# Kernel optimization log

Hardware: AMD Instinct MI355X
Metric: run time of the kernel (lower is better)

## Reference

```python
import jax, jax.numpy as jnp
import numpy as np

N = 50000      # nodes
E = 640000     # edges (before self loops)
IN = 128       # in_channels
H = 4          # heads (layer 1)
C = 64         # hidden_channels per head
OUT = 64       # out_channels
SLOPE = 0.2    # PyG GATConv default negative_slope


def setup_inputs() -> dict:
    key = jax.random.key(0)
    ks = jax.random.split(key, 12)
    x = jax.random.normal(ks[0], (N, IN), dtype=jnp.float32)
    edge_src = jax.random.randint(ks[1], (E,), 0, N, dtype=jnp.int32)
    edge_dst = jax.random.randint(ks[2], (E,), 0, N, dtype=jnp.int32)
    # Layer 1 params: Linear IN -> H*C, attention vectors a_src/a_dst [H, C], bias [H*C]
    W1 = jax.random.normal(ks[3], (IN, H * C), dtype=jnp.float32) / np.sqrt(IN)
    att_src1 = jax.random.normal(ks[4], (H, C), dtype=jnp.float32) / np.sqrt(C)
    att_dst1 = jax.random.normal(ks[5], (H, C), dtype=jnp.float32) / np.sqrt(C)
    b1 = jnp.zeros((H * C,), dtype=jnp.float32)
    # Layer 2 params: Linear H*C -> OUT, 1 head
    W2 = jax.random.normal(ks[6], (H * C, OUT), dtype=jnp.float32) / np.sqrt(H * C)
    att_src2 = jax.random.normal(ks[7], (1, OUT), dtype=jnp.float32) / np.sqrt(OUT)
    att_dst2 = jax.random.normal(ks[8], (1, OUT), dtype=jnp.float32) / np.sqrt(OUT)
    b2 = jnp.zeros((OUT,), dtype=jnp.float32)
    return {"x": x, "W1": W1, "att_src1": att_src1, "att_dst1": att_dst1, "b1": b1,
            "W2": W2, "att_src2": att_src2, "att_dst2": att_dst2, "b2": b2,
            "edge_src": edge_src, "edge_dst": edge_dst}


def gat_conv(x, src, dst, W, a_src, a_dst, b, heads, ch):
    """PyG GATConv (concat=True): gather -> LeakyReLU attention -> per-dst softmax -> scatter-add."""
    n = x.shape[0]
    h = (x @ W).reshape(n, heads, ch)                  # [N, H, C]
    al_s = jnp.sum(h * a_src, axis=-1)                 # [N, H] node-level src attention term
    al_d = jnp.sum(h * a_dst, axis=-1)                 # [N, H]
    e = jax.nn.leaky_relu(al_s[src] + al_d[dst], SLOPE)  # [E, H] edge scores
    m = jax.ops.segment_max(e, dst, num_segments=n)    # stable per-dst softmax
    ex = jnp.exp(e - m[dst])
    den = jax.ops.segment_sum(ex, dst, num_segments=n)
    alpha = ex / den[dst]                              # [E, H]
    msg = h[src] * alpha[:, :, None]                   # [E, H, C]
    out = jax.ops.segment_sum(msg, dst, num_segments=n)  # [N, H, C]
    return out.reshape(n, heads * ch) + b


def reference(x, W1, att_src1, att_dst1, b1, W2, att_src2, att_dst2, b2, edge_src, edge_dst):
    # PyG GATConv default add_self_loops=True
    loops = jnp.arange(N, dtype=edge_src.dtype)
    src = jnp.concatenate([edge_src, loops])
    dst = jnp.concatenate([edge_dst, loops])
    h = gat_conv(x, src, dst, W1, att_src1, att_dst1, b1, H, C)
    h = jax.nn.elu(h)                                  # F.elu; dropout p=0 -> no-op
    out = gat_conv(h, src, dst, W2, att_src2, att_dst2, b2, 1, OUT)
    return out
```

## Files before the change

kernel.cpp:

```cpp
#include <hip/hip_runtime.h>
#include <hip/hip_bf16.h>
#include <cstdint>
#include <cstddef>

#define N_NODES 50000
#define N_EDGES 640000
#define ET (N_EDGES + N_NODES)
#define IN_CH 128
#define H1 4
#define HC1 256
#define OUT_CH 64
#define SLOPE 0.2f
#define SCAN_NBLK ((N_NODES + 255) / 256)

typedef __attribute__((ext_vector_type(8))) short short8;
typedef __attribute__((ext_vector_type(4))) float floatx4;

__device__ __forceinline__ float bf2f(unsigned short u) {
    return __uint_as_float(((unsigned)u) << 16);
}
__device__ __forceinline__ unsigned short f2bf(float f) {
    unsigned u = __float_as_uint(f);
    unsigned r = 0x7fffu + ((u >> 16) & 1u);
    return (unsigned short)((u + r) >> 16);
}
__device__ __forceinline__ float ldf(const void* p, size_t i, bool f32) {
    return f32 ? ((const float*)p)[i] : bf2f(((const unsigned short*)p)[i]);
}

__global__ void detect_dtype(const unsigned short* __restrict__ x, unsigned* __restrict__ flag) {
    if (blockIdx.x == 0 && threadIdx.x == 0) {
        int bad = 0;
        for (int i = 0; i < 256; ++i) {
            float v = bf2f(x[i]);
            if (!(v == v) || fabsf(v) > 1e4f) bad++;
        }
        *flag = (bad > 0) ? 1u : 0u;
    }
}

__global__ void conv_x(const void* __restrict__ x, const unsigned* __restrict__ flag,
                       unsigned short* __restrict__ x16)
{
    int i = blockIdx.x * blockDim.x + threadIdx.x;
    if (i >= N_NODES * IN_CH / 8) return;
    size_t off = (size_t)i * 8;
    uint4 st;
    if (*flag) {
        const float* xp = (const float*)x + off;
        float4 a = *(const float4*)xp;
        float4 b = *(const float4*)(xp + 4);
        st.x = (unsigned)f2bf(a.x) | ((unsigned)f2bf(a.y) << 16);
        st.y = (unsigned)f2bf(a.z) | ((unsigned)f2bf(a.w) << 16);
        st.z = (unsigned)f2bf(b.x) | ((unsigned)f2bf(b.y) << 16);
        st.w = (unsigned)f2bf(b.z) | ((unsigned)f2bf(b.w) << 16);
    } else {
        st = *(const uint4*)((const unsigned short*)x + off);
    }
    *(uint4*)(x16 + off) = st;
}

__global__ void conv_w(const void* __restrict__ W, const unsigned* __restrict__ flag,
                       unsigned short* __restrict__ Wt, int K, int N)
{
    int i = blockIdx.x * blockDim.x + threadIdx.x;
    if (i >= N * K) return;
    int n = i / K, k = i % K;
    Wt[i] = f2bf(ldf(W, (size_t)k * N + n, *flag != 0));
}

__global__ void count_edges(const int* __restrict__ edst, int* __restrict__ counts)
{
    int i = blockIdx.x * blockDim.x + threadIdx.x;
    if (i >= ET) return;
    int d = (i < N_EDGES) ? edst[i] : (i - N_EDGES);
    atomicAdd(&counts[d], 1);
}

__global__ __launch_bounds__(256) void block_sums(
    const int* __restrict__ counts, int* __restrict__ bsum)
{
    int i = blockIdx.x * 256 + threadIdx.x;
    int v = (i < N_NODES) ? counts[i] : 0;
    #pragma unroll
    for (int off = 32; off > 0; off >>= 1) v += __shfl_down(v, off, 64);
    __shared__ int ws[4];
    int lane = threadIdx.x & 63, w = threadIdx.x >> 6;
    if (lane == 0) ws[w] = v;
    __syncthreads();
    if (threadIdx.x == 0) bsum[blockIdx.x] = ws[0] + ws[1] + ws[2] + ws[3];
}

__global__ __launch_bounds__(256) void scan_block_sums(
    const int* __restrict__ bsum, int* __restrict__ boff)
{
    __shared__ int s[256];
    int t = threadIdx.x;
    int v = (t < SCAN_NBLK) ? bsum[t] : 0;
    s[t] = v;
    __syncthreads();
    #pragma unroll
    for (int off = 1; off < 256; off <<= 1) {
        int u = (t >= off) ? s[t - off] : 0;
        __syncthreads();
        s[t] += u;
        __syncthreads();
    }
    if (t < SCAN_NBLK) boff[t] = s[t] - v;
}

__global__ __launch_bounds__(256) void write_rowptr(
    const int* __restrict__ counts, const int* __restrict__ boff,
    int* __restrict__ rowptr, int* __restrict__ cursor)
{
    __shared__ int s[256];
    int t = threadIdx.x;
    int i = blockIdx.x * 256 + t;
    int v = (i < N_NODES) ? counts[i] : 0;
    s[t] = v;
    __syncthreads();
    #pragma unroll
    for (int off = 1; off < 256; off <<= 1) {
        int u = (t >= off) ? s[t - off] : 0;
        __syncthreads();
        s[t] += u;
        __syncthreads();
    }
    if (i < N_NODES) {
        int r = boff[blockIdx.x] + s[t] - v;
        rowptr[i] = r; cursor[i] = r;
    }
    if (i == 0) rowptr[N_NODES] = ET;
}

__global__ void fill_csr(const int* __restrict__ esrc, const int* __restrict__ edst,
                         int* __restrict__ cursor, int* __restrict__ ecsr)
{
    int i = blockIdx.x * blockDim.x + threadIdx.x;
    if (i >= ET) return;
    int s = (i < N_EDGES) ? esrc[i] : (i - N_EDGES);
    int d = (i < N_EDGES) ? edst[i] : (i - N_EDGES);
    int pos = atomicAdd(&cursor[d], 1);
    ecsr[pos] = s;
}

template <int KK>
__global__ __launch_bounds__(256) void gemm_fused(
    const unsigned short* __restrict__ A,
    const unsigned short* __restrict__ Bt,
    const void* __restrict__ avs, const void* __restrict__ avd,
    const unsigned* __restrict__ flag,
    unsigned short* __restrict__ C,
    float* __restrict__ als, float* __restrict__ ald,
    int M, int N)
{
    const int tid = threadIdx.x;
    const int m0 = blockIdx.y * 64, n0 = blockIdx.x * 64;
    const int w = tid >> 6, lane = tid & 63;
    const int ln = lane & 15, quad = lane >> 4;
    const int m_frag = m0 + w * 16 + ln;
    floatx4 acc[4] = {{0.f,0.f,0.f,0.f},{0.f,0.f,0.f,0.f},{0.f,0.f,0.f,0.f},{0.f,0.f,0.f,0.f}};

    #pragma unroll
    for (int ks = 0; ks < KK / 32; ++ks) {
        const int kbase = ks * 32 + quad * 8;
        short8 a;
        if (m_frag < M) {
            a = *(const short8*)(A + (size_t)m_frag * KK + kbase);
        } else {
            #pragma unroll
            for (int j = 0; j < 8; ++j) a[j] = 0;
        }
        #pragma unroll
        for (int sub = 0; sub < 4; ++sub) {
            short8 b = *(const short8*)(Bt + (size_t)(n0 + sub * 16 + ln) * KK + kbase);
            acc[sub] = __builtin_amdgcn_mfma_f32_16x16x32_bf16(a, b, acc[sub], 0, 0, 0);
        }
    }

    #pragma unroll
    for (int sub = 0; sub < 4; ++sub) {
        #pragma unroll
        for (int r = 0; r < 4; ++r) {
            int m = m0 + w * 16 + quad * 4 + r;
            if (m < M)
                C[(size_t)m * N + n0 + sub * 16 + ln] = f2bf(acc[sub][r]);
        }
    }

    const bool f32in = (*flag != 0);
    float as[4], av[4];
    #pragma unroll
    for (int sub = 0; sub < 4; ++sub) {
        as[sub] = ldf(avs, n0 + sub * 16 + ln, f32in);
        av[sub] = ldf(avd, n0 + sub * 16 + ln, f32in);
    }
    const int Hh = N >> 6;
    #pragma unroll
    for (int r = 0; r < 4; ++r) {
        float ps = 0.f, pd = 0.f;
        #pragma unroll
        for (int sub = 0; sub < 4; ++sub) {
            ps += acc[sub][r] * as[sub];
            pd += acc[sub][r] * av[sub];
        }
        #pragma unroll
        for (int off = 1; off < 16; off <<= 1) {
            ps += __shfl_xor(ps, off, 64);
            pd += __shfl_xor(pd, off, 64);
        }
        int m = m0 + w * 16 + quad * 4 + r;
        if (ln == 0 && m < M) {
            als[(size_t)m * Hh + blockIdx.x] = ps;
            ald[(size_t)m * Hh + blockIdx.x] = pd;
        }
    }
}

__global__ __launch_bounds__(256) void agg_node1(
    const int* __restrict__ rowptr, const int* __restrict__ ecsr,
    const unsigned short* __restrict__ h, const float* __restrict__ als,
    const float* __restrict__ ald, const void* __restrict__ bias,
    const unsigned* __restrict__ flag, unsigned short* __restrict__ out)
{
    int wave = (blockIdx.x * blockDim.x + threadIdx.x) >> 6;
    int lane = threadIdx.x & 63;
    if (wave >= N_NODES) return;
    const int d = wave;
    const int hg = lane >> 4;
    const int c0 = (lane & 15) << 2;
    const int lo = rowptr[d], hi = rowptr[d + 1];
    const float ad = ald[d * H1 + hg];

    float acc0 = 0.f, acc1 = 0.f, acc2 = 0.f, acc3 = 0.f, den = 0.f;

    int e = lo;
    for (; e + 1 < hi; e += 2) {
        int s0 = ecsr[e], s1 = ecsr[e + 1];
        uint2 q0 = *(const uint2*)(h + (size_t)s0 * HC1 + hg * 64 + c0);
        uint2 q1 = *(const uint2*)(h + (size_t)s1 * HC1 + hg * 64 + c0);
        float t0 = als[s0 * H1 + hg] + ad;
        float t1 = als[s1 * H1 + hg] + ad;
        t0 = (t0 > 0.f) ? t0 : SLOPE * t0;
        t1 = (t1 > 0.f) ? t1 : SLOPE * t1;
        float p0 = __expf(t0), p1 = __expf(t1);
        den += p0 + p1;
        acc0 += p0 * __uint_as_float(q0.x << 16)         + p1 * __uint_as_float(q1.x << 16);
        acc1 += p0 * __uint_as_float(q0.x & 0xffff0000u) + p1 * __uint_as_float(q1.x & 0xffff0000u);
        acc2 += p0 * __uint_as_float(q0.y << 16)         + p1 * __uint_as_float(q1.y << 16);
        acc3 += p0 * __uint_as_float(q0.y & 0xffff0000u) + p1 * __uint_as_float(q1.y & 0xffff0000u);
    }
    if (e < hi) {
        int s0 = ecsr[e];
        uint2 q0 = *(const uint2*)(h + (size_t)s0 * HC1 + hg * 64 + c0);
        float t0 = als[s0 * H1 + hg] + ad;
        t0 = (t0 > 0.f) ? t0 : SLOPE * t0;
        float p0 = __expf(t0);
        den += p0;
        acc0 += p0 * __uint_as_float(q0.x << 16);
        acc1 += p0 * __uint_as_float(q0.x & 0xffff0000u);
        acc2 += p0 * __uint_as_float(q0.y << 16);
        acc3 += p0 * __uint_as_float(q0.y & 0xffff0000u);
    }

    const bool f32in = (*flag != 0);
    const float inv = 1.f / den;
    float v0 = acc0 * inv + ldf(bias, hg * 64 + c0 + 0, f32in);
    float v1 = acc1 * inv + ldf(bias, hg * 64 + c0 + 1, f32in);
    float v2 = acc2 * inv + ldf(bias, hg * 64 + c0 + 2, f32in);
    float v3 = acc3 * inv + ldf(bias, hg * 64 + c0 + 3, f32in);
    v0 = (v0 > 0.f) ? v0 : (__expf(v0) - 1.f);
    v1 = (v1 > 0.f) ? v1 : (__expf(v1) - 1.f);
    v2 = (v2 > 0.f) ? v2 : (__expf(v2) - 1.f);
    v3 = (v3 > 0.f) ? v3 : (__expf(v3) - 1.f);
    uint2 st;
    st.x = (unsigned)f2bf(v0) | ((unsigned)f2bf(v1) << 16);
    st.y = (unsigned)f2bf(v2) | ((unsigned)f2bf(v3) << 16);
    *(uint2*)(out + (size_t)d * HC1 + hg * 64 + c0) = st;
}

__global__ __launch_bounds__(256) void agg_node2(
    const int* __restrict__ rowptr, const int* __restrict__ ecsr,
    const unsigned short* __restrict__ h, const float* __restrict__ als,
    const float* __restrict__ ald, const void* __restrict__ bias,
    const unsigned* __restrict__ flag, float* __restrict__ out)
{
    int wave = (blockIdx.x * blockDim.x + threadIdx.x) >> 6;
    int lane = threadIdx.x & 63;
    if (wave >= N_NODES) return;
    const int d = wave;
    const int eg = lane >> 4;
    const int c0 = (lane & 15) << 2;
    const int lo = rowptr[d], hi = rowptr[d + 1];
    const float ad = ald[d];

    float acc0 = 0.f, acc1 = 0.f, acc2 = 0.f, acc3 = 0.f, den = 0.f;

    for (int eb = lo; eb < hi; eb += 4) {
        int e = eb + eg;
        if (e < hi) {
            int s = ecsr[e];
            uint2 q = *(const uint2*)(h + (size_t)s * OUT_CH + c0);
            float t = als[s] + ad;
            t = (t > 0.f) ? t : SLOPE * t;
            float p = __expf(t);
            den += p;
            acc0 += p * __uint_as_float(q.x << 16);
            acc1 += p * __uint_as_float(q.x & 0xffff0000u);
            acc2 += p * __uint_as_float(q.y << 16);
            acc3 += p * __uint_as_float(q.y & 0xffff0000u);
        }
    }
    #pragma unroll
    for (int off = 16; off <= 32; off <<= 1) {
        den  += __shfl_xor(den,  off, 64);
        acc0 += __shfl_xor(acc0, off, 64);
        acc1 += __shfl_xor(acc1, off, 64);
        acc2 += __shfl_xor(acc2, off, 64);
        acc3 += __shfl_xor(acc3, off, 64);
    }
    if (lane < 16) {
        const bool f32in = (*flag != 0);
        const float inv = 1.f / den;
        float4 v;
        v.x = acc0 * inv + ldf(bias, c0 + 0, f32in);
        v.y = acc1 * inv + ldf(bias, c0 + 1, f32in);
        v.z = acc2 * inv + ldf(bias, c0 + 2, f32in);
        v.w = acc3 * inv + ldf(bias, c0 + 3, f32in);
        *(float4*)(out + (size_t)d * OUT_CH + c0) = v;
    }
}

extern "C" void kernel_launch(void* const* d_in, const int* in_sizes, int n_in,
                              void* d_out, int out_size, void* d_ws, size_t ws_size,
                              hipStream_t stream)
{
    const void* x   = d_in[0];
    const void* W1  = d_in[1];
    const void* as1 = d_in[2];
    const void* ad1 = d_in[3];
    const void* b1  = d_in[4];
    const void* W2  = d_in[5];
    const void* as2 = d_in[6];
    const void* ad2 = d_in[7];
    const void* b2  = d_in[8];
    const int* esrc = (const int*)d_in[9];
    const int* edst = (const int*)d_in[10];
    float* out = (float*)d_out;

    char* base = (char*)d_ws;
    const size_t MB = 1024 * 1024;
    unsigned short* x16  = (unsigned short*)(base);
    unsigned short* h16  = (unsigned short*)(base + 13 * MB);
    unsigned short* xo16 = (unsigned short*)(base + 39 * MB);
    unsigned short* h2   = (unsigned short*)(base + 65 * MB);
    float* als    = (float*)(base + 72 * MB);
    float* ald    = (float*)(base + 73 * MB);
    unsigned short* Wt1 = (unsigned short*)(base + 74 * MB);
    unsigned short* Wt2 = (unsigned short*)(base + 75 * MB);
    int* counts   = (int*)(base + 76 * MB);
    int* rowptr   = (int*)(base + 77 * MB);
    int* cursor   = (int*)(base + 78 * MB);
    int* ecsr     = (int*)(base + 79 * MB);
    int* bsum     = (int*)(base + 82 * MB);
    int* boff     = bsum + 256;
    unsigned* flag = (unsigned*)(base + 83 * MB);

    const int BLK = 256;
    const int edge_blocks = (ET + BLK - 1) / BLK;
    const int node_wave_blocks = (N_NODES * 64 + BLK - 1) / BLK;

    detect_dtype<<<1, 64, 0, stream>>>((const unsigned short*)x, flag);

    (void)hipMemsetAsync(counts, 0, N_NODES * sizeof(int), stream);
    count_edges<<<edge_blocks, BLK, 0, stream>>>(edst, counts);
    block_sums<<<SCAN_NBLK, BLK, 0, stream>>>(counts, bsum);
    scan_block_sums<<<1, BLK, 0, stream>>>(bsum, boff);
    write_rowptr<<<SCAN_NBLK, BLK, 0, stream>>>(counts, boff, rowptr, cursor);
    fill_csr<<<edge_blocks, BLK, 0, stream>>>(esrc, edst, cursor, ecsr);

    conv_x<<<(N_NODES * IN_CH / 8 + BLK - 1) / BLK, BLK, 0, stream>>>(x, flag, x16);
    conv_w<<<(IN_CH * HC1 + BLK - 1) / BLK, BLK, 0, stream>>>(W1, flag, Wt1, IN_CH, HC1);
    conv_w<<<(HC1 * OUT_CH + BLK - 1) / BLK, BLK, 0, stream>>>(W2, flag, Wt2, HC1, OUT_CH);

    {
        dim3 g(HC1 / 64, (N_NODES + 63) / 64);
        gemm_fused<IN_CH><<<g, BLK, 0, stream>>>(x16, Wt1, as1, ad1, flag, h16, als, ald, N_NODES, HC1);
    }
    agg_node1<<<node_wave_blocks, BLK, 0, stream>>>(
        rowptr, ecsr, h16, als, ald, b1, flag, xo16);

    {
        dim3 g(OUT_CH / 64, (N_NODES + 63) / 64);
        gemm_fused<HC1><<<g, BLK, 0, stream>>>(xo16, Wt2, as2, ad2, flag, h2, als, ald, N_NODES, OUT_CH);
    }
    agg_node2<<<node_wave_blocks, BLK, 0, stream>>>(
        rowptr, ecsr, h2, als, ald, b2, flag, out);
}
```

Baseline: 325.4 us.

## Compute all heads per GEMM block, unroll layer-1 aggregation, widen layer-2 loads

Layer-1 GEMM now runs one block per 64-row tile covering all four heads, so each A fragment is loaded once instead of once per column tile, at the cost of 64 accumulator registers per thread. The layer-1 aggregation loop is unrolled to four edges per iteration to keep more gathers in flight. Layer-2 aggregation switches to 8 edge groups of 8 lanes, each loading 16-byte rows, which adds one more shuffle reduction stage. The layer-2 GEMM drops its N-tiling parameters and becomes single-tile.

```diff
diff --git a/kernel.cpp b/kernel.cpp
--- a/kernel.cpp
+++ b/kernel.cpp
@@ -144,6 +144,91 @@
     ecsr[pos] = s;
 }
 
+__global__ __launch_bounds__(256) void gemm_fused4(
+    const unsigned short* __restrict__ A,
+    const unsigned short* __restrict__ Bt,
+    const void* __restrict__ avs, const void* __restrict__ avd,
+    const unsigned* __restrict__ flag,
+    unsigned short* __restrict__ C,
+    float* __restrict__ als, float* __restrict__ ald,
+    int M)
+{
+    const int tid = threadIdx.x;
+    const int m0 = blockIdx.x * 64;
+    const int w = tid >> 6, lane = tid & 63;
+    const int ln = lane & 15, quad = lane >> 4;
+    const int m_frag = m0 + w * 16 + ln;
+    floatx4 acc[4][4];
+    #pragma unroll
+    for (int hh = 0; hh < 4; ++hh)
+        #pragma unroll
+        for (int sub = 0; sub < 4; ++sub)
+            acc[hh][sub] = (floatx4){0.f, 0.f, 0.f, 0.f};
+
+    #pragma unroll
+    for (int ks = 0; ks < IN_CH / 32; ++ks) {
+        const int kbase = ks * 32 + quad * 8;
+        short8 a;
+        if (m_frag < M) {
+            a = *(const short8*)(A + (size_t)m_frag * IN_CH + kbase);
+        } else {
+            #pragma unroll
+            for (int j = 0; j < 8; ++j) a[j] = 0;
+        }
+        #pragma unroll
+        for (int hh = 0; hh < 4; ++hh) {
+            #pragma unroll
+            for (int sub = 0; sub < 4; ++sub) {
+                short8 b = *(const short8*)(Bt + (size_t)(hh * 64 + sub * 16 + ln) * IN_CH + kbase);
+                acc[hh][sub] = __builtin_amdgcn_mfma_f32_16x16x32_bf16(a, b, acc[hh][sub], 0, 0, 0);
+            }
+        }
+    }
+
+    #pragma unroll
+    for (int hh = 0; hh < 4; ++hh) {
+        #pragma unroll
+        for (int sub = 0; sub < 4; ++sub) {
+            #pragma unroll
+            for (int r = 0; r < 4; ++r) {
+                int m = m0 + w * 16 + quad * 4 + r;
+                if (m < M)
+                    C[(size_t)m * HC1 + hh * 64 + sub * 16 + ln] = f2bf(acc[hh][sub][r]);
+            }
+        }
+    }
+
+    const bool f32in = (*flag != 0);
+    #pragma unroll
+    for (int hh = 0; hh < 4; ++hh) {
+        float as[4], av[4];
+        #pragma unroll
+        for (int sub = 0; sub < 4; ++sub) {
+            as[sub] = ldf(avs, hh * 64 + sub * 16 + ln, f32in);
+            av[sub] = ldf(avd, hh * 64 + sub * 16 + ln, f32in);
+        }
+        #pragma unroll
+        for (int r = 0; r < 4; ++r) {
+            float ps = 0.f, pd = 0.f;
+            #pragma unroll
+            for (int sub = 0; sub < 4; ++sub) {
+                ps += acc[hh][sub][r] * as[sub];
+                pd += acc[hh][sub][r] * av[sub];
+            }
+            #pragma unroll
+            for (int off = 1; off < 16; off <<= 1) {
+                ps += __shfl_xor(ps, off, 64);
+                pd += __shfl_xor(pd, off, 64);
+            }
+            int m = m0 + w * 16 + quad * 4 + r;
+            if (ln == 0 && m < M) {
+                als[(size_t)m * H1 + hh] = ps;
+                ald[(size_t)m * H1 + hh] = pd;
+            }
+        }
+    }
+}
+
 template <int KK>
 __global__ __launch_bounds__(256) void gemm_fused(
     const unsigned short* __restrict__ A,
@@ -152,10 +237,10 @@
     const unsigned* __restrict__ flag,
     unsigned short* __restrict__ C,
     float* __restrict__ als, float* __restrict__ ald,
-    int M, int N)
+    int M)
 {
     const int tid = threadIdx.x;
-    const int m0 = blockIdx.y * 64, n0 = blockIdx.x * 64;
+    const int m0 = blockIdx.x * 64;
     const int w = tid >> 6, lane = tid & 63;
     const int ln = lane & 15, quad = lane >> 4;
     const int m_frag = m0 + w * 16 + ln;
@@ -173,7 +258,7 @@
         }
         #pragma unroll
         for (int sub = 0; sub < 4; ++sub) {
-            short8 b = *(const short8*)(Bt + (size_t)(n0 + sub * 16 + ln) * KK + kbase);
+            short8 b = *(const short8*)(Bt + (size_t)(sub * 16 + ln) * KK + kbase);
             acc[sub] = __builtin_amdgcn_mfma_f32_16x16x32_bf16(a, b, acc[sub], 0, 0, 0);
         }
     }
@@ -184,7 +269,7 @@
         for (int r = 0; r < 4; ++r) {
             int m = m0 + w * 16 + quad * 4 + r;
             if (m < M)
-                C[(size_t)m * N + n0 + sub * 16 + ln] = f2bf(acc[sub][r]);
+                C[(size_t)m * OUT_CH + sub * 16 + ln] = f2bf(acc[sub][r]);
         }
     }
 
@@ -192,10 +277,9 @@
     float as[4], av[4];
     #pragma unroll
     for (int sub = 0; sub < 4; ++sub) {
-        as[sub] = ldf(avs, n0 + sub * 16 + ln, f32in);
-        av[sub] = ldf(avd, n0 + sub * 16 + ln, f32in);
-    }
-    const int Hh = N >> 6;
+        as[sub] = ldf(avs, sub * 16 + ln, f32in);
+        av[sub] = ldf(avd, sub * 16 + ln, f32in);
+    }
     #pragma unroll
     for (int r = 0; r < 4; ++r) {
         float ps = 0.f, pd = 0.f;
@@ -211,8 +295,8 @@
         }
         int m = m0 + w * 16 + quad * 4 + r;
         if (ln == 0 && m < M) {
-            als[(size_t)m * Hh + blockIdx.x] = ps;
-            ald[(size_t)m * Hh + blockIdx.x] = pd;
+            als[m] = ps;
+            ald[m] = pd;
         }
     }
 }
@@ -235,22 +319,32 @@
     float acc0 = 0.f, acc1 = 0.f, acc2 = 0.f, acc3 = 0.f, den = 0.f;
 
     int e = lo;
-    for (; e + 1 < hi; e += 2) {
-        int s0 = ecsr[e], s1 = ecsr[e + 1];
+    for (; e + 3 < hi; e += 4) {
+        int s0 = ecsr[e], s1 = ecsr[e + 1], s2 = ecsr[e + 2], s3 = ecsr[e + 3];
         uint2 q0 = *(const uint2*)(h + (size_t)s0 * HC1 + hg * 64 + c0);
         uint2 q1 = *(const uint2*)(h + (size_t)s1 * HC1 + hg * 64 + c0);
+        uint2 q2 = *(const uint2*)(h + (size_t)s2 * HC1 + hg * 64 + c0);
+        uint2 q3 = *(const uint2*)(h + (size_t)s3 * HC1 + hg * 64 + c0);
         float t0 = als[s0 * H1 + hg] + ad;
         float t1 = als[s1 * H1 + hg] + ad;
+        float t2 = als[s2 * H1 + hg] + ad;
+        float t3 = als[s3 * H1 + hg] + ad;
         t0 = (t0 > 0.f) ? t0 : SLOPE * t0;
         t1 = (t1 > 0.f) ? t1 : SLOPE * t1;
-        float p0 = __expf(t0), p1 = __expf(t1);
-        den += p0 + p1;
-        acc0 += p0 * __uint_as_float(q0.x << 16)         + p1 * __uint_as_float(q1.x << 16);
-        acc1 += p0 * __uint_as_float(q0.x & 0xffff0000u) + p1 * __uint_as_float(q1.x & 0xffff0000u);
-        acc2 += p0 * __uint_as_float(q0.y << 16)         + p1 * __uint_as_float(q1.y << 16);
-        acc3 += p0 * __uint_as_float(q0.y & 0xffff0000u) + p1 * __uint_as_float(q1.y & 0xffff0000u);
-    }
-    if (e < hi) {
+        t2 = (t2 > 0.f) ? t2 : SLOPE * t2;
+        t3 = (t3 > 0.f) ? t3 : SLOPE * t3;
+        float p0 = __expf(t0), p1 = __expf(t1), p2 = __expf(t2), p3 = __expf(t3);
+        den += (p0 + p1) + (p2 + p3);
+        acc0 += p0 * __uint_as_float(q0.x << 16)         + p1 * __uint_as_float(q1.x << 16)
+              + p2 * __uint_as_float(q2.x << 16)         + p3 * __uint_as_float(q3.x << 16);
+        acc1 += p0 * __uint_as_float(q0.x & 0xffff0000u) + p1 * __uint_as_float(q1.x & 0xffff0000u)
+              + p2 * __uint_as_float(q2.x & 0xffff0000u) + p3 * __uint_as_float(q3.x & 0xffff0000u);
+        acc2 += p0 * __uint_as_float(q0.y << 16)         + p1 * __uint_as_float(q1.y << 16)
+              + p2 * __uint_as_float(q2.y << 16)         + p3 * __uint_as_float(q3.y << 16);
+        acc3 += p0 * __uint_as_float(q0.y & 0xffff0000u) + p1 * __uint_as_float(q1.y & 0xffff0000u)
+              + p2 * __uint_as_float(q2.y & 0xffff0000u) + p3 * __uint_as_float(q3.y & 0xffff0000u);
+    }
+    for (; e < hi; ++e) {
         int s0 = ecsr[e];
         uint2 q0 = *(const uint2*)(h + (size_t)s0 * HC1 + hg * 64 + c0);
         float t0 = als[s0 * H1 + hg] + ad;
@@ -289,45 +383,55 @@
     int lane = threadIdx.x & 63;
     if (wave >= N_NODES) return;
     const int d = wave;
-    const int eg = lane >> 4;
-    const int c0 = (lane & 15) << 2;
+    const int eg = lane >> 3;
+    const int c0 = (lane & 7) << 3;
     const int lo = rowptr[d], hi = rowptr[d + 1];
     const float ad = ald[d];
 
-    float acc0 = 0.f, acc1 = 0.f, acc2 = 0.f, acc3 = 0.f, den = 0.f;
-
-    for (int eb = lo; eb < hi; eb += 4) {
+    float acc[8];
+    #pragma unroll
+    for (int j = 0; j < 8; ++j) acc[j] = 0.f;
+    float den = 0.f;
+
+    for (int eb = lo; eb < hi; eb += 8) {
         int e = eb + eg;
         if (e < hi) {
             int s = ecsr[e];
-            uint2 q = *(const uint2*)(h + (size_t)s * OUT_CH + c0);
+            uint4 q = *(const uint4*)(h + (size_t)s * OUT_CH + c0);
             float t = als[s] + ad;
             t = (t > 0.f) ? t : SLOPE * t;
             float p = __expf(t);
             den += p;
-            acc0 += p * __uint_as_float(q.x << 16);
-            acc1 += p * __uint_as_float(q.x & 0xffff0000u);
-            acc2 += p * __uint_as_float(q.y << 16);
-            acc3 += p * __uint_as_float(q.y & 0xffff0000u);
-        }
-    }
-    #pragma unroll
-    for (int off = 16; off <= 32; off <<= 1) {
-        den  += __shfl_xor(den,  off, 64);
-        acc0 += __shfl_xor(acc0, off, 64);
-        acc1 += __shfl_xor(acc1, off, 64);
-        acc2 += __shfl_xor(acc2, off, 64);
-        acc3 += __shfl_xor(acc3, off, 64);
-    }
-    if (lane < 16) {
+            acc[0] += p * __uint_as_float(q.x << 16);
+            acc[1] += p * __uint_as_float(q.x & 0xffff0000u);
+            acc[2] += p * __uint_as_float(q.y << 16);
+            acc[3] += p * __uint_as_float(q.y & 0xffff0000u);
+            acc[4] += p * __uint_as_float(q.z << 16);
+            acc[5] += p * __uint_as_float(q.z & 0xffff0000u);
+            acc[6] += p * __uint_as_float(q.w << 16);
+            acc[7] += p * __uint_as_float(q.w & 0xffff0000u);
+        }
+    }
+    #pragma unroll
+    for (int off = 8; off <= 32; off <<= 1) {
+        den += __shfl_xor(den, off, 64);
+        #pragma unroll
+        for (int j = 0; j < 8; ++j) acc[j] += __shfl_xor(acc[j], off, 64);
+    }
+    if (lane < 8) {
         const bool f32in = (*flag != 0);
         const float inv = 1.f / den;
-        float4 v;
-        v.x = acc0 * inv + ldf(bias, c0 + 0, f32in);
-        v.y = acc1 * inv + ldf(bias, c0 + 1, f32in);
-        v.z = acc2 * inv + ldf(bias, c0 + 2, f32in);
-        v.w = acc3 * inv + ldf(bias, c0 + 3, f32in);
-        *(float4*)(out + (size_t)d * OUT_CH + c0) = v;
+        float4 v0, v1;
+        v0.x = acc[0] * inv + ldf(bias, c0 + 0, f32in);
+        v0.y = acc[1] * inv + ldf(bias, c0 + 1, f32in);
+        v0.z = acc[2] * inv + ldf(bias, c0 + 2, f32in);
+        v0.w = acc[3] * inv + ldf(bias, c0 + 3, f32in);
+        v1.x = acc[4] * inv + ldf(bias, c0 + 4, f32in);
+        v1.y = acc[5] * inv + ldf(bias, c0 + 5, f32in);
+        v1.z = acc[6] * inv + ldf(bias, c0 + 6, f32in);
+        v1.w = acc[7] * inv + ldf(bias, c0 + 7, f32in);
+        *(float4*)(out + (size_t)d * OUT_CH + c0) = v0;
+        *(float4*)(out + (size_t)d * OUT_CH + c0 + 4) = v1;
     }
 }
 
@@ -369,6 +473,7 @@
     const int BLK = 256;
     const int edge_blocks = (ET + BLK - 1) / BLK;
     const int node_wave_blocks = (N_NODES * 64 + BLK - 1) / BLK;
+    const int mtiles = (N_NODES + 63) / 64;
 
     detect_dtype<<<1, 64, 0, stream>>>((const unsigned short*)x, flag);
 
@@ -383,17 +488,11 @@
     conv_w<<<(IN_CH * HC1 + BLK - 1) / BLK, BLK, 0, stream>>>(W1, flag, Wt1, IN_CH, HC1);
     conv_w<<<(HC1 * OUT_CH + BLK - 1) / BLK, BLK, 0, stream>>>(W2, flag, Wt2, HC1, OUT_CH);
 
-    {
-        dim3 g(HC1 / 64, (N_NODES + 63) / 64);
-        gemm_fused<IN_CH><<<g, BLK, 0, stream>>>(x16, Wt1, as1, ad1, flag, h16, als, ald, N_NODES, HC1);
-    }
+    gemm_fused4<<<mtiles, BLK, 0, stream>>>(x16, Wt1, as1, ad1, flag, h16, als, ald, N_NODES);
     agg_node1<<<node_wave_blocks, BLK, 0, stream>>>(
         rowptr, ecsr, h16, als, ald, b1, flag, xo16);
 
-    {
-        dim3 g(OUT_CH / 64, (N_NODES + 63) / 64);
-        gemm_fused<HC1><<<g, BLK, 0, stream>>>(xo16, Wt2, as2, ad2, flag, h2, als, ald, N_NODES, OUT_CH);
-    }
+    gemm_fused<HC1><<<mtiles, BLK, 0, stream>>>(xo16, Wt2, as2, ad2, flag, h2, als, ald, N_NODES);
     agg_node2<<<node_wave_blocks, BLK, 0, stream>>>(
         rowptr, ecsr, h2, als, ald, b2, flag, out);
 }
```

Measured after the change: 327.3 us. No clear change (+0.6%).

## Batch gathers in aggregation, widen layer-2 lanes, fuse conversion kernels

Applied to the files above, without the earlier changes.

The layer-1 aggregation now loads eight neighbour indices at once, then issues all eight feature gathers before doing any math. This raises memory-level parallelism; out-of-range slots are clamped and given zero weight. The layer-2 aggregation switches to 8 edge groups of 8 lanes, each loading 16-byte vectors, and reduces across three shuffle stages. The x, W1 and W2 conversion kernels are merged into one launch, and dtype detection uses a wave ballot. These changes add register pressure and wasted loads for low-degree nodes.

```diff
diff --git a/kernel.cpp b/kernel.cpp
--- a/kernel.cpp
+++ b/kernel.cpp
@@ -29,44 +29,51 @@
 }
 
 __global__ void detect_dtype(const unsigned short* __restrict__ x, unsigned* __restrict__ flag) {
-    if (blockIdx.x == 0 && threadIdx.x == 0) {
-        int bad = 0;
-        for (int i = 0; i < 256; ++i) {
-            float v = bf2f(x[i]);
-            if (!(v == v) || fabsf(v) > 1e4f) bad++;
-        }
-        *flag = (bad > 0) ? 1u : 0u;
-    }
-}
-
-__global__ void conv_x(const void* __restrict__ x, const unsigned* __restrict__ flag,
-                       unsigned short* __restrict__ x16)
+    int lane = threadIdx.x & 63;
+    int bad = 0;
+    #pragma unroll
+    for (int r = 0; r < 4; ++r) {
+        float v = bf2f(x[r * 64 + lane]);
+        if (!(v == v) || fabsf(v) > 1e4f) bad = 1;
+    }
+    unsigned long long m = __ballot(bad != 0);
+    if (lane == 0) *flag = (m != 0ull) ? 1u : 0u;
+}
+
+#define XW (N_NODES * IN_CH / 8)
+#define W1N (IN_CH * HC1)
+#define W2N (HC1 * OUT_CH)
+__global__ void conv_all(const void* __restrict__ x, const void* __restrict__ W1,
+                         const void* __restrict__ W2, const unsigned* __restrict__ flag,
+                         unsigned short* __restrict__ x16,
+                         unsigned short* __restrict__ Wt1, unsigned short* __restrict__ Wt2)
 {
     int i = blockIdx.x * blockDim.x + threadIdx.x;
-    if (i >= N_NODES * IN_CH / 8) return;
-    size_t off = (size_t)i * 8;
-    uint4 st;
-    if (*flag) {
-        const float* xp = (const float*)x + off;
-        float4 a = *(const float4*)xp;
-        float4 b = *(const float4*)(xp + 4);
-        st.x = (unsigned)f2bf(a.x) | ((unsigned)f2bf(a.y) << 16);
-        st.y = (unsigned)f2bf(a.z) | ((unsigned)f2bf(a.w) << 16);
-        st.z = (unsigned)f2bf(b.x) | ((unsigned)f2bf(b.y) << 16);
-        st.w = (unsigned)f2bf(b.z) | ((unsigned)f2bf(b.w) << 16);
-    } else {
-        st = *(const uint4*)((const unsigned short*)x + off);
-    }
-    *(uint4*)(x16 + off) = st;
-}
-
-__global__ void conv_w(const void* __restrict__ W, const unsigned* __restrict__ flag,
-                       unsigned short* __restrict__ Wt, int K, int N)
-{
-    int i = blockIdx.x * blockDim.x + threadIdx.x;
-    if (i >= N * K) return;
-    int n = i / K, k = i % K;
-    Wt[i] = f2bf(ldf(W, (size_t)k * N + n, *flag != 0));
+    const bool f32 = (*flag != 0);
+    if (i < XW) {
+        size_t off = (size_t)i * 8;
+        uint4 st;
+        if (f32) {
+            const float* xp = (const float*)x + off;
+            float4 a = *(const float4*)xp;
+            float4 b = *(const float4*)(xp + 4);
+            st.x = (unsigned)f2bf(a.x) | ((unsigned)f2bf(a.y) << 16);
+            st.y = (unsigned)f2bf(a.z) | ((unsigned)f2bf(a.w) << 16);
+            st.z = (unsigned)f2bf(b.x) | ((unsigned)f2bf(b.y) << 16);
+            st.w = (unsigned)f2bf(b.z) | ((unsigned)f2bf(b.w) << 16);
+        } else {
+            st = *(const uint4*)((const unsigned short*)x + off);
+        }
+        *(uint4*)(x16 + off) = st;
+    } else if (i < XW + W1N) {
+        int j = i - XW;
+        int n = j / IN_CH, k = j % IN_CH;
+        Wt1[j] = f2bf(ldf(W1, (size_t)k * HC1 + n, f32));
+    } else if (i < XW + W1N + W2N) {
+        int j = i - XW - W1N;
+        int n = j / HC1, k = j % HC1;
+        Wt2[j] = f2bf(ldf(W2, (size_t)k * OUT_CH + n, f32));
+    }
 }
 
 __global__ void count_edges(const int* __restrict__ edst, int* __restrict__ counts)
@@ -234,33 +241,31 @@
 
     float acc0 = 0.f, acc1 = 0.f, acc2 = 0.f, acc3 = 0.f, den = 0.f;
 
-    int e = lo;
-    for (; e + 1 < hi; e += 2) {
-        int s0 = ecsr[e], s1 = ecsr[e + 1];
-        uint2 q0 = *(const uint2*)(h + (size_t)s0 * HC1 + hg * 64 + c0);
-        uint2 q1 = *(const uint2*)(h + (size_t)s1 * HC1 + hg * 64 + c0);
-        float t0 = als[s0 * H1 + hg] + ad;
-        float t1 = als[s1 * H1 + hg] + ad;
-        t0 = (t0 > 0.f) ? t0 : SLOPE * t0;
-        t1 = (t1 > 0.f) ? t1 : SLOPE * t1;
-        float p0 = __expf(t0), p1 = __expf(t1);
-        den += p0 + p1;
-        acc0 += p0 * __uint_as_float(q0.x << 16)         + p1 * __uint_as_float(q1.x << 16);
-        acc1 += p0 * __uint_as_float(q0.x & 0xffff0000u) + p1 * __uint_as_float(q1.x & 0xffff0000u);
-        acc2 += p0 * __uint_as_float(q0.y << 16)         + p1 * __uint_as_float(q1.y << 16);
-        acc3 += p0 * __uint_as_float(q0.y & 0xffff0000u) + p1 * __uint_as_float(q1.y & 0xffff0000u);
-    }
-    if (e < hi) {
-        int s0 = ecsr[e];
-        uint2 q0 = *(const uint2*)(h + (size_t)s0 * HC1 + hg * 64 + c0);
-        float t0 = als[s0 * H1 + hg] + ad;
-        t0 = (t0 > 0.f) ? t0 : SLOPE * t0;
-        float p0 = __expf(t0);
-        den += p0;
-        acc0 += p0 * __uint_as_float(q0.x << 16);
-        acc1 += p0 * __uint_as_float(q0.x & 0xffff0000u);
-        acc2 += p0 * __uint_as_float(q0.y << 16);
-        acc3 += p0 * __uint_as_float(q0.y & 0xffff0000u);
+    for (int eb = lo; eb < hi; eb += 8) {
+        int s[8]; uint2 q[8]; float p[8];
+        #pragma unroll
+        for (int j = 0; j < 8; ++j) {
+            int e = eb + j;
+            s[j] = ecsr[(e < hi) ? e : (hi - 1)];
+        }
+        #pragma unroll
+        for (int j = 0; j < 8; ++j)
+            q[j] = *(const uint2*)(h + (size_t)s[j] * HC1 + hg * 64 + c0);
+        #pragma unroll
+        for (int j = 0; j < 8; ++j) {
+            float t = als[s[j] * H1 + hg] + ad;
+            t = (t > 0.f) ? t : SLOPE * t;
+            float pv = __expf(t);
+            p[j] = (eb + j < hi) ? pv : 0.f;
+        }
+        #pragma unroll
+        for (int j = 0; j < 8; ++j) {
+            den  += p[j];
+            acc0 += p[j] * __uint_as_float(q[j].x << 16);
+            acc1 += p[j] * __uint_as_float(q[j].x & 0xffff0000u);
+            acc2 += p[j] * __uint_as_float(q[j].y << 16);
+            acc3 += p[j] * __uint_as_float(q[j].y & 0xffff0000u);
+        }
     }
 
     const bool f32in = (*flag != 0);
@@ -289,45 +294,55 @@
     int lane = threadIdx.x & 63;
     if (wave >= N_NODES) return;
     const int d = wave;
-    const int eg = lane >> 4;
-    const int c0 = (lane & 15) << 2;
+    const int eg = lane >> 3;
+    const int c0 = (lane & 7) << 3;
     const int lo = rowptr[d], hi = rowptr[d + 1];
     const float ad = ald[d];
 
-    float acc0 = 0.f, acc1 = 0.f, acc2 = 0.f, acc3 = 0.f, den = 0.f;
-
-    for (int eb = lo; eb < hi; eb += 4) {
+    float acc[8];
+    #pragma unroll
+    for (int j = 0; j < 8; ++j) acc[j] = 0.f;
+    float den = 0.f;
+
+    for (int eb = lo; eb < hi; eb += 8) {
         int e = eb + eg;
         if (e < hi) {
             int s = ecsr[e];
-            uint2 q = *(const uint2*)(h + (size_t)s * OUT_CH + c0);
+            uint4 q = *(const uint4*)(h + (size_t)s * OUT_CH + c0);
             float t = als[s] + ad;
             t = (t > 0.f) ? t : SLOPE * t;
             float p = __expf(t);
             den += p;
-            acc0 += p * __uint_as_float(q.x << 16);
-            acc1 += p * __uint_as_float(q.x & 0xffff0000u);
-            acc2 += p * __uint_as_float(q.y << 16);
-            acc3 += p * __uint_as_float(q.y & 0xffff0000u);
-        }
-    }
-    #pragma unroll
-    for (int off = 16; off <= 32; off <<= 1) {
-        den  += __shfl_xor(den,  off, 64);
-        acc0 += __shfl_xor(acc0, off, 64);
-        acc1 += __shfl_xor(acc1, off, 64);
-        acc2 += __shfl_xor(acc2, off, 64);
-        acc3 += __shfl_xor(acc3, off, 64);
-    }
-    if (lane < 16) {
+            acc[0] += p * __uint_as_float(q.x << 16);
+            acc[1] += p * __uint_as_float(q.x & 0xffff0000u);
+            acc[2] += p * __uint_as_float(q.y << 16);
+            acc[3] += p * __uint_as_float(q.y & 0xffff0000u);
+            acc[4] += p * __uint_as_float(q.z << 16);
+            acc[5] += p * __uint_as_float(q.z & 0xffff0000u);
+            acc[6] += p * __uint_as_float(q.w << 16);
+            acc[7] += p * __uint_as_float(q.w & 0xffff0000u);
+        }
+    }
+    #pragma unroll
+    for (int off = 8; off <= 32; off <<= 1) {
+        den += __shfl_xor(den, off, 64);
+        #pragma unroll
+        for (int j = 0; j < 8; ++j) acc[j] += __shfl_xor(acc[j], off, 64);
+    }
+    if (lane < 8) {
         const bool f32in = (*flag != 0);
         const float inv = 1.f / den;
-        float4 v;
-        v.x = acc0 * inv + ldf(bias, c0 + 0, f32in);
-        v.y = acc1 * inv + ldf(bias, c0 + 1, f32in);
-        v.z = acc2 * inv + ldf(bias, c0 + 2, f32in);
-        v.w = acc3 * inv + ldf(bias, c0 + 3, f32in);
-        *(float4*)(out + (size_t)d * OUT_CH + c0) = v;
+        float4 v0, v1;
+        v0.x = acc[0] * inv + ldf(bias, c0 + 0, f32in);
+        v0.y = acc[1] * inv + ldf(bias, c0 + 1, f32in);
+        v0.z = acc[2] * inv + ldf(bias, c0 + 2, f32in);
+        v0.w = acc[3] * inv + ldf(bias, c0 + 3, f32in);
+        v1.x = acc[4] * inv + ldf(bias, c0 + 4, f32in);
+        v1.y = acc[5] * inv + ldf(bias, c0 + 5, f32in);
+        v1.z = acc[6] * inv + ldf(bias, c0 + 6, f32in);
+        v1.w = acc[7] * inv + ldf(bias, c0 + 7, f32in);
+        *(float4*)(out + (size_t)d * OUT_CH + c0) = v0;
+        *(float4*)(out + (size_t)d * OUT_CH + c0 + 4) = v1;
     }
 }
 
@@ -369,6 +384,7 @@
     const int BLK = 256;
     const int edge_blocks = (ET + BLK - 1) / BLK;
     const int node_wave_blocks = (N_NODES * 64 + BLK - 1) / BLK;
+    const int mtiles = (N_NODES + 63) / 64;
 
     detect_dtype<<<1, 64, 0, stream>>>((const unsigned short*)x, flag);
 
@@ -379,19 +395,18 @@
     write_rowptr<<<SCAN_NBLK, BLK, 0, stream>>>(counts, boff, rowptr, cursor);
     fill_csr<<<edge_blocks, BLK, 0, stream>>>(esrc, edst, cursor, ecsr);
 
-    conv_x<<<(N_NODES * IN_CH / 8 + BLK - 1) / BLK, BLK, 0, stream>>>(x, flag, x16);
-    conv_w<<<(IN_CH * HC1 + BLK - 1) / BLK, BLK, 0, stream>>>(W1, flag, Wt1, IN_CH, HC1);
-    conv_w<<<(HC1 * OUT_CH + BLK - 1) / BLK, BLK, 0, stream>>>(W2, flag, Wt2, HC1, OUT_CH);
+    conv_all<<<(XW + W1N + W2N + BLK - 1) / BLK, BLK, 0, stream>>>(
+        x, W1, W2, flag, x16, Wt1, Wt2);
 
     {
-        dim3 g(HC1 / 64, (N_NODES + 63) / 64);
+        dim3 g(HC1 / 64, mtiles);
         gemm_fused<IN_CH><<<g, BLK, 0, stream>>>(x16, Wt1, as1, ad1, flag, h16, als, ald, N_NODES, HC1);
     }
     agg_node1<<<node_wave_blocks, BLK, 0, stream>>>(
         rowptr, ecsr, h16, als, ald, b1, flag, xo16);
 
     {
-        dim3 g(OUT_CH / 64, (N_NODES + 63) / 64);
+        dim3 g(OUT_CH / 64, mtiles);
         gemm_fused<HC1><<<g, BLK, 0, stream>>>(xo16, Wt2, as2, ad2, flag, h2, als, ald, N_NODES, OUT_CH);
     }
     agg_node2<<<node_wave_blocks, BLK, 0, stream>>>(
```

Result: faster. 307.8 us (-5.4%).
